# Kernel tuning notes

Hardware: AMD Instinct MI355X
Metric: run time of the kernel (lower is better)

The kernel has to match this reference:

```python
import jax, jax.numpy as jnp
import numpy as np
from functools import partial

N = 100_000   # nodes
E = 1_600_000 # edges (avg degree 16)
C = 128       # hidden channels
H = 4         # heads
D = C // H    # head dim = 32
L = 2         # layers
OUT = 2       # out channels


def setup_inputs() -> dict:
    key = jax.random.key(0)
    ks = jax.random.split(key, 12)
    s = 1.0 / np.sqrt(C)
    sd = 1.0 / np.sqrt(D)
    inp = {
        "x": jax.random.normal(ks[0], (N, C), jnp.float32),
        "edge_index": jax.random.randint(ks[1], (2, E), 0, N, jnp.int64),
        "Wk": jax.random.normal(ks[2], (L, C, C), jnp.float32) * s,
        "bk": jnp.zeros((L, C), jnp.float32),
        "Wq": jax.random.normal(ks[3], (L, C, C), jnp.float32) * s,
        "bq": jnp.zeros((L, C), jnp.float32),
        "Wv": jax.random.normal(ks[4], (L, C, C), jnp.float32) * s,
        "bv": jnp.zeros((L, C), jnp.float32),
        "a_rel": jax.random.normal(ks[5], (L, H, D, D), jnp.float32) * sd,
        "m_rel": jax.random.normal(ks[6], (L, H, D, D), jnp.float32) * sd,
        "p_rel": jnp.ones((L, H), jnp.float32),
        "Wa": jax.random.normal(ks[7], (L, C, C), jnp.float32) * s,
        "ba": jnp.zeros((L, C), jnp.float32),
        "skip": jnp.ones((L,), jnp.float32),
        "Wfc": jax.random.normal(ks[8], (C, OUT), jnp.float32) * s,
        "bfc": jnp.zeros((OUT,), jnp.float32),
    }
    return inp


def _hgt_layer(x, src, dst, Wk, bk, Wq, bq, Wv, bv, a_rel, m_rel, p_rel, Wa, ba, skip):
    n = x.shape[0]
    k = (x @ Wk + bk).reshape(n, H, D)
    q = (x @ Wq + bq).reshape(n, H, D)
    v = (x @ Wv + bv).reshape(n, H, D)
    # relation-specific transforms (single edge type)
    k = jnp.einsum('nhd,hde->nhe', k, a_rel)
    v = jnp.einsum('nhd,hde->nhe', v, m_rel)
    # per-edge attention logits [E, H]
    alpha = jnp.einsum('ehd,ehd->eh', q[dst], k[src]) * p_rel / np.sqrt(D)
    # segment softmax over incoming edges of each dst node
    amax = jax.ops.segment_max(alpha, dst, num_segments=n)
    ez = jnp.exp(alpha - amax[dst])
    denom = jax.ops.segment_sum(ez, dst, num_segments=n)
    attn = ez / denom[dst]
    # weighted messages -> scatter-sum to dst
    msg = (v[src] * attn[:, :, None]).reshape(-1, C)  # [E, C]
    agg = jax.ops.segment_sum(msg, dst, num_segments=n)  # [N, C]
    out = jax.nn.gelu(agg, approximate=False) @ Wa + ba
    g = jax.nn.sigmoid(skip)
    return g * out + (1.0 - g) * x


def reference(x, edge_index, Wk, bk, Wq, bq, Wv, bv, a_rel, m_rel, p_rel, Wa, ba, skip, Wfc, bfc):
    src, dst = edge_index[0], edge_index[1]
    h = x
    for l in range(L):
        h = _hgt_layer(h, src, dst, Wk[l], bk[l], Wq[l], bq[l], Wv[l], bv[l],
                       a_rel[l], m_rel[l], p_rel[l], Wa[l], ba[l], skip[l])
    return h @ Wfc + bfc
```

## Files before the change

### kernel.cpp

```cpp
#include <hip/hip_runtime.h>
#include <hip/hip_bf16.h>
#include <math.h>

#define CD 128
#define HH 4
#define DH 32
#define LL 2

using bf16 = __hip_bfloat16;
using bf16x8 = __attribute__((ext_vector_type(8))) short;
using f32x4 = __attribute__((ext_vector_type(4))) float;

__device__ __forceinline__ float bfbits2f(unsigned int s) {
  return __uint_as_float(s << 16);
}

__device__ __forceinline__ unsigned short f2bfbits(float f) {
  unsigned int u = __float_as_uint(f);
  unsigned int r = (u + 0x7fff + ((u >> 16) & 1)) >> 16;
  return (unsigned short)r;
}

__device__ __forceinline__ float gelu_f(float x) {
  return 0.5f * x * (1.0f + erff(x * 0.70710678118654752f));
}

__global__ void k_detect(const void* __restrict__ x, const int* __restrict__ ei,
                         int* __restrict__ flags) {
  __shared__ int cnt_f32, cnt_i32;
  if (threadIdx.x == 0) { cnt_f32 = 0; cnt_i32 = 0; }
  __syncthreads();
  int t = threadIdx.x;
  unsigned short u = ((const unsigned short*)x)[2 * t];
  float v = bfbits2f((unsigned int)u);
  float av = fabsf(v);
  if (av != 0.f && (av > 1e8f || av < 1e-8f)) atomicAdd(&cnt_f32, 1);
  if (t < 64) {
    if (((const int*)ei)[2 * t + 1] != 0) atomicAdd(&cnt_i32, 1);
  }
  __syncthreads();
  if (threadIdx.x == 0) {
    flags[0] = (cnt_f32 > 8) ? 1 : 0;
    flags[1] = (cnt_i32 == 0) ? 1 : 0;
  }
}

#define NSEG 14
struct SegTab {
  const void* src[NSEG];
  int off[NSEG];
  int total;
};

__device__ __forceinline__ int edge_idx(const int* __restrict__ ei, long pos, int is64) {
  return is64 ? ei[2 * pos] : ei[pos];
}

#define BTILE 4096

__global__ __launch_bounds__(256) void k_pre(
    SegTab tab, float* __restrict__ pdst,
    const int* __restrict__ ei, int* __restrict__ deg, int* __restrict__ bcnt,
    int E, int Nn, int shift, const int* __restrict__ flags, int parB) {
  __shared__ int cnt[256];
  const int bx = blockIdx.x;
  if (bx < parB) {
    int i = bx * 256 + threadIdx.x;
    if (i >= tab.total) return;
    int seg = 0;
#pragma unroll
    for (int k = 1; k < NSEG; k++)
      if (i >= tab.off[k]) seg = k;
    int j = i - tab.off[seg];
    const void* src = tab.src[seg];
    pdst[i] = flags[0] ? ((const float*)src)[j]
                       : bfbits2f((unsigned int)((const unsigned short*)src)[j]);
  } else {
    cnt[threadIdx.x] = 0;
    __syncthreads();
    const int t0 = (bx - parB) * BTILE;
    const int is64 = flags[1];
    for (int j = 0; j < 16; j++) {
      int i = t0 + threadIdx.x + j * 256;
      if (i < E) {
        int d = edge_idx(ei, (long)E + i, is64);
        if ((unsigned)d >= (unsigned)Nn) d = 0;
        atomicAdd(&deg[d], 1);
        atomicAdd(&cnt[d >> shift], 1);
      }
    }
    __syncthreads();
    int v = cnt[threadIdx.x];
    if (v > 0) atomicAdd(&bcnt[threadIdx.x], v);
  }
}

__global__ __launch_bounds__(256) void k_w1(
    const float* __restrict__ pWk, const float* __restrict__ pbk,
    const float* __restrict__ pWv, const float* __restrict__ pbv,
    const float* __restrict__ par, const float* __restrict__ pmr,
    unsigned short* __restrict__ wkeT, float* __restrict__ bke,
    unsigned short* __restrict__ wveT, float* __restrict__ bve,
    const float* __restrict__ pWq, const float* __restrict__ pWa,
    unsigned short* __restrict__ wqT, unsigned short* __restrict__ waT,
    const int* __restrict__ deg, int* __restrict__ tmp, int* __restrict__ bsum,
    int n, int effB, int wtB) {
  __shared__ int sh[256];
  const int bx = blockIdx.x;
  if (bx < effB) {
    int i = bx * 256 + threadIdx.x;
    const int total = LL * 2 * (CD + 1) * HH * DH;
    if (i >= total) return;
    int e = i & 31;
    int h = (i >> 5) & 3;
    int c = (i >> 7) % (CD + 1);
    int z = (i >> 7) / (CD + 1);
    int l = z >> 1, which = z & 1;
    const float* W = (which ? pWv : pWk) + (size_t)l * CD * CD;
    const float* B = (which ? pbv : pbk) + (size_t)l * CD;
    const float* R = (which ? pmr : par) + (size_t)l * HH * DH * DH + h * DH * DH;
    unsigned short* WoT = (which ? wveT : wkeT) + (size_t)l * CD * CD;
    float* Bo = (which ? bve : bke) + (size_t)l * CD;
    float acc = 0.f;
    if (c < CD) {
#pragma unroll
      for (int d = 0; d < DH; d++) acc += W[c * CD + h * DH + d] * R[d * DH + e];
      WoT[(size_t)(h * DH + e) * CD + c] = f2bfbits(acc);
    } else {
#pragma unroll
      for (int d = 0; d < DH; d++) acc += B[h * DH + d] * R[d * DH + e];
      Bo[h * DH + e] = acc;
    }
  } else if (bx < effB + wtB) {
    int i = (bx - effB) * 256 + threadIdx.x;
    int cin = i & 127;
    int cout = (i >> 7) & 127;
    int z = i >> 14;
    int l = z >> 1, which = z & 1;
    const float* W = (which ? pWa : pWq) + (size_t)l * CD * CD;
    unsigned short* WT = (which ? waT : wqT) + (size_t)l * CD * CD;
    WT[(size_t)cout * CD + cin] = f2bfbits(W[(size_t)cin * CD + cout]);
  } else {
    const int b = bx - effB - wtB;
    int i = b * 256 + threadIdx.x;
    int v = (i < n) ? deg[i] : 0;
    sh[threadIdx.x] = v;
    __syncthreads();
    for (int off = 1; off < 256; off <<= 1) {
      int t = (threadIdx.x >= off) ? sh[threadIdx.x - off] : 0;
      __syncthreads();
      sh[threadIdx.x] += t;
      __syncthreads();
    }
    if (i < n) tmp[i] = sh[threadIdx.x];
    if (threadIdx.x == 255) bsum[b] = sh[255];
  }
}

__global__ __launch_bounds__(256) void k_s2(
    int* __restrict__ bsum, int nb, const int* __restrict__ bcnt,
    int* __restrict__ bbase, int* __restrict__ bfill) {
  __shared__ int sh[256];
  __shared__ int carry;
  if (blockIdx.x == 0) {
    if (threadIdx.x == 0) carry = 0;
    __syncthreads();
    for (int base = 0; base < nb; base += 256) {
      int i = base + threadIdx.x;
      int v = (i < nb) ? bsum[i] : 0;
      sh[threadIdx.x] = v;
      __syncthreads();
      for (int off = 1; off < 256; off <<= 1) {
        int t = (threadIdx.x >= off) ? sh[threadIdx.x - off] : 0;
        __syncthreads();
        sh[threadIdx.x] += t;
        __syncthreads();
      }
      if (i < nb) bsum[i] = sh[threadIdx.x] + carry;
      __syncthreads();
      if (threadIdx.x == 0) carry += sh[255];
      __syncthreads();
    }
  } else {
    int t = threadIdx.x;
    int v = bcnt[t];
    sh[t] = v;
    __syncthreads();
    for (int off = 1; off < 256; off <<= 1) {
      int u = (t >= off) ? sh[t - off] : 0;
      __syncthreads();
      sh[t] += u;
      __syncthreads();
    }
    int excl = sh[t] - v;
    bbase[t] = excl;
    bfill[t] = excl;
  }
}

__global__ __launch_bounds__(256) void k_s3bin(
    const int* __restrict__ tmp, const int* __restrict__ deg,
    const int* __restrict__ bsum, int* __restrict__ rowptr,
    int* __restrict__ fill, int n, int nB,
    const int* __restrict__ ei, int* __restrict__ bfill,
    int* __restrict__ ebs, int* __restrict__ ebd,
    const int* __restrict__ flags, int E, int Nn, int shift) {
  __shared__ int sS[BTILE];
  __shared__ int sD[BTILE];
  __shared__ int cnt[256], pref[256], base[256], lofs[256];
  const int bx = blockIdx.x;
  if (bx < nB) {
    int i = bx * 256 + threadIdx.x;
    if (i >= n) return;
    int off = (bx > 0) ? bsum[bx - 1] : 0;
    int excl = tmp[i] - deg[i] + off;
    rowptr[i] = excl;
    fill[i] = excl;
    return;
  }
  const int t = threadIdx.x;
  cnt[t] = 0;
  lofs[t] = 0;
  __syncthreads();
  const int t0 = (bx - nB) * BTILE;
  const int is64 = flags[1];
  for (int j = 0; j < 16; j++) {
    int i = t0 + t + j * 256;
    if (i < E) {
      int d = edge_idx(ei, (long)E + i, is64);
      if ((unsigned)d >= (unsigned)Nn) d = 0;
      atomicAdd(&cnt[d >> shift], 1);
    }
  }
  __syncthreads();
  {
    int v = cnt[t];
    pref[t] = v;
    __syncthreads();
    for (int off = 1; off < 256; off <<= 1) {
      int u = (t >= off) ? pref[t - off] : 0;
      __syncthreads();
      pref[t] += u;
      __syncthreads();
    }
    int incl = pref[t];
    __syncthreads();
    pref[t] = incl - v;
    base[t] = (v > 0) ? atomicAdd(&bfill[t], v) : 0;
  }
  __syncthreads();
  for (int j = 0; j < 16; j++) {
    int i = t0 + t + j * 256;
    if (i < E) {
      int s = edge_idx(ei, (long)i, is64);
      int d = edge_idx(ei, (long)E + i, is64);
      if ((unsigned)s >= (unsigned)Nn) s = 0;
      if ((unsigned)d >= (unsigned)Nn) d = 0;
      int b = d >> shift;
      int p = pref[b] + atomicAdd(&lofs[b], 1);
      sS[p] = s;
      sD[p] = d;
    }
  }
  __syncthreads();
  int tot = E - t0;
  if (tot > BTILE) tot = BTILE;
  for (int j = 0; j < 16; j++) {
    int i = t + j * 256;
    if (i < tot) {
      int d = sD[i];
      int b = d >> shift;
      int gp = base[b] + (i - pref[b]);
      ebs[gp] = sS[i];
      ebd[gp] = d;
    }
  }
}

__global__ void k_scatter2(const int* __restrict__ bbase, const int* __restrict__ bcnt,
                           const int* __restrict__ ebs, const int* __restrict__ ebd,
                           int* __restrict__ fill, int* __restrict__ csr_src) {
  int b = blockIdx.x >> 1, half = blockIdx.x & 1;
  int s0 = bbase[b], c = bcnt[b];
  int st = s0 + (half ? (c + 1) / 2 : 0);
  int en = s0 + (half ? c : (c + 1) / 2);
  for (int i = st + threadIdx.x; i < en; i += 256) {
    int s = ebs[i], d = ebd[i];
    int pos = atomicAdd(&fill[d], 1);
    csr_src[pos] = s;
  }
}

__global__ __launch_bounds__(256, 4) void k_gemm_qkv(
    const void* __restrict__ Araw, int a_is_x, const int* __restrict__ flags,
    const unsigned short* __restrict__ wq, const unsigned short* __restrict__ wk,
    const unsigned short* __restrict__ wv,
    const float* __restrict__ bq, const float* __restrict__ bk,
    const float* __restrict__ bv,
    float* __restrict__ qout, unsigned short* __restrict__ kvout, int nrows) {
  const int which = blockIdx.y;
  const unsigned short* BT = (which == 0) ? wq : (which == 1) ? wk : wv;
  const float* bias = (which == 0) ? bq : (which == 1) ? bk : bv;
  const int w = threadIdx.x >> 6;
  const int l = threadIdx.x & 63;
  const int r0 = blockIdx.x * 64 + w * 16;
  if (r0 >= nrows) return;
  const int lrow = l & 15;
  const int quad = l >> 4;
  const int k0 = quad * 8;
  const int ax_f32 = a_is_x ? flags[0] : 0;

  f32x4 acc[8];
#pragma unroll
  for (int ct = 0; ct < 8; ct++) {
    float b = bias[ct * 16 + lrow];
    acc[ct] = (f32x4){b, b, b, b};
  }
  int ar = r0 + lrow;
  if (ar >= nrows) ar = nrows - 1;
#pragma unroll
  for (int kc = 0; kc < 4; kc++) {
    bf16x8 af;
    if (ax_f32) {
      const float* Af = (const float*)Araw + (size_t)ar * CD + kc * 32 + k0;
      float4 a = *(const float4*)Af;
      float4 b = *(const float4*)(Af + 4);
      af[0] = (short)f2bfbits(a.x); af[1] = (short)f2bfbits(a.y);
      af[2] = (short)f2bfbits(a.z); af[3] = (short)f2bfbits(a.w);
      af[4] = (short)f2bfbits(b.x); af[5] = (short)f2bfbits(b.y);
      af[6] = (short)f2bfbits(b.z); af[7] = (short)f2bfbits(b.w);
    } else {
      af = *(const bf16x8*)((const unsigned short*)Araw + (size_t)ar * CD + kc * 32 + k0);
    }
#pragma unroll
    for (int ct = 0; ct < 8; ct++) {
      bf16x8 bfr = *(const bf16x8*)(BT + (size_t)(ct * 16 + lrow) * CD + kc * 32 + k0);
      acc[ct] = __builtin_amdgcn_mfma_f32_16x16x32_bf16(af, bfr, acc[ct], 0, 0, 0);
    }
  }
#pragma unroll
  for (int ct = 0; ct < 8; ct++) {
#pragma unroll
    for (int i = 0; i < 4; i++) {
      int gr = r0 + quad * 4 + i;
      if (gr >= nrows) continue;
      int col = ct * 16 + lrow;
      float val = acc[ct][i];
      if (which == 0) {
        qout[(size_t)gr * CD + col] = val;
      } else {
        unsigned short* o = kvout + ((size_t)gr << 8) + ((which == 2) ? CD : 0);
        o[col] = f2bfbits(val);
      }
    }
  }
}

__global__ __launch_bounds__(256, 3) void k_gate_qkv(
    const unsigned short* __restrict__ A, const unsigned short* __restrict__ BTa,
    const float* __restrict__ ba, const void* __restrict__ xres,
    float* __restrict__ h, const float* __restrict__ skip,
    const int* __restrict__ flags,
    const unsigned short* __restrict__ wq1, const unsigned short* __restrict__ wk1,
    const unsigned short* __restrict__ wv1,
    const float* __restrict__ bq1, const float* __restrict__ bk1,
    const float* __restrict__ bv1,
    float* __restrict__ qout, unsigned short* __restrict__ kvout, int nrows) {
  __shared__ unsigned short sA[64][136];
  __shared__ unsigned short sW[128 * 128];
  const int t = threadIdx.x;
  const int w = t >> 6;
  const int l = t & 63;
  const int blkbase = blockIdx.x * 64;
  const int r0 = blkbase + w * 16;
  const int lrow = l & 15;
  const int quad = l >> 4;
  const int k0 = quad * 8;
  const int xf32 = flags[0];
  const bool act = (r0 < nrows);
  const int srow = t >> 1;
  const int shf = t & 1;

  {
    const unsigned short* src = BTa + (size_t)srow * CD + shf * 64;
#pragma unroll
    for (int j = 0; j < 8; j++) {
      int c = shf * 8 + j;
      int cs = c ^ (srow & 15);
      *(uint4*)(&sW[srow * 128 + cs * 8]) = *(const uint4*)(src + j * 8);
    }
  }
  __syncthreads();

  if (act) {
    f32x4 acc[8];
#pragma unroll
    for (int ct = 0; ct < 8; ct++) {
      float b = ba[ct * 16 + lrow];
      acc[ct] = (f32x4){b, b, b, b};
    }
    int ar = r0 + lrow;
    if (ar >= nrows) ar = nrows - 1;
    const unsigned short* Ap = A + (size_t)ar * CD;
#pragma unroll
    for (int kc = 0; kc < 4; kc++) {
      bf16x8 af = *(const bf16x8*)(Ap + kc * 32 + k0);
#pragma unroll
      for (int ct = 0; ct < 8; ct++) {
        int cs = (kc * 4 + quad) ^ lrow;
        bf16x8 bfr = *(const bf16x8*)(&sW[(ct * 16 + lrow) * 128 + cs * 8]);
        acc[ct] = __builtin_amdgcn_mfma_f32_16x16x32_bf16(af, bfr, acc[ct], 0, 0, 0);
      }
    }
    float gg = 1.f / (1.f + __expf(-skip[0]));
#pragma unroll
    for (int ct = 0; ct < 8; ct++) {
#pragma unroll
      for (int i = 0; i < 4; i++) {
        int gr = r0 + quad * 4 + i;
        if (gr >= nrows) continue;
        size_t ix = (size_t)gr * CD + ct * 16 + lrow;
        float hres = xf32 ? ((const float*)xres)[ix]
                          : bfbits2f((unsigned int)((const unsigned short*)xres)[ix]);
        float o = gg * acc[ct][i] + (1.f - gg) * hres;
        h[ix] = o;
        sA[gr - blkbase][ct * 16 + lrow] = f2bfbits(o);
      }
    }
  }
  __syncthreads();

  int ar = r0 + lrow;
  if (ar >= nrows) ar = nrows - 1;
  const unsigned short* Alds = &sA[ar - blkbase][0];
#pragma unroll 1
  for (int which = 0; which < 3; which++) {
    const unsigned short* BT = (which == 0) ? wq1 : (which == 1) ? wk1 : wv1;
    const float* bias = (which == 0) ? bq1 : (which == 1) ? bk1 : bv1;
    {
      const unsigned short* src = BT + (size_t)srow * CD + shf * 64;
#pragma unroll
      for (int j = 0; j < 8; j++) {
        int c = shf * 8 + j;
        int cs = c ^ (srow & 15);
        *(uint4*)(&sW[srow * 128 + cs * 8]) = *(const uint4*)(src + j * 8);
      }
    }
    __syncthreads();
    if (act) {
      f32x4 acc[8];
#pragma unroll
      for (int ct = 0; ct < 8; ct++) {
        float b = bias[ct * 16 + lrow];
        acc[ct] = (f32x4){b, b, b, b};
      }
#pragma unroll
      for (int kc = 0; kc < 4; kc++) {
        bf16x8 af = *(const bf16x8*)(Alds + kc * 32 + k0);
#pragma unroll
        for (int ct = 0; ct < 8; ct++) {
          int cs = (kc * 4 + quad) ^ lrow;
          bf16x8 bfr = *(const bf16x8*)(&sW[(ct * 16 + lrow) * 128 + cs * 8]);
          acc[ct] = __builtin_amdgcn_mfma_f32_16x16x32_bf16(af, bfr, acc[ct], 0, 0, 0);
        }
      }
#pragma unroll
      for (int ct = 0; ct < 8; ct++) {
#pragma unroll
        for (int i = 0; i < 4; i++) {
          int gr = r0 + quad * 4 + i;
          if (gr >= nrows) continue;
          int col = ct * 16 + lrow;
          float val = acc[ct][i];
          if (which == 0) {
            qout[(size_t)gr * CD + col] = val;
          } else {
            unsigned short* o = kvout + ((size_t)gr << 8) + ((which == 2) ? CD : 0);
            o[col] = f2bfbits(val);
          }
        }
      }
    }
    __syncthreads();
  }
}

__global__ __launch_bounds__(256, 4) void k_gemm_gate(
    const unsigned short* __restrict__ A, const unsigned short* __restrict__ BT,
    const float* __restrict__ bias, const float* __restrict__ h,
    const float* __restrict__ skip,
    const float* __restrict__ Wfc, const float* __restrict__ bfc,
    void* __restrict__ out, const int* __restrict__ flags, int nrows) {
  const int w = threadIdx.x >> 6;
  const int l = threadIdx.x & 63;
  const int r0 = blockIdx.x * 64 + w * 16;
  if (r0 >= nrows) return;
  const int lrow = l & 15;
  const int quad = l >> 4;
  const int k0 = quad * 8;
  const int xf32 = flags[0];

  f32x4 acc[8];
#pragma unroll
  for (int ct = 0; ct < 8; ct++) {
    float b = bias[ct * 16 + lrow];
    acc[ct] = (f32x4){b, b, b, b};
  }
  int ar = r0 + lrow;
  if (ar >= nrows) ar = nrows - 1;
  const unsigned short* Ap = A + (size_t)ar * CD;
#pragma unroll
  for (int kc = 0; kc < 4; kc++) {
    bf16x8 af = *(const bf16x8*)(Ap + kc * 32 + k0);
#pragma unroll
    for (int ct = 0; ct < 8; ct++) {
      bf16x8 bfr = *(const bf16x8*)(BT + (size_t)(ct * 16 + lrow) * CD + kc * 32 + k0);
      acc[ct] = __builtin_amdgcn_mfma_f32_16x16x32_bf16(af, bfr, acc[ct], 0, 0, 0);
    }
  }
  float gg = 1.f / (1.f + __expf(-skip[0]));
  float p0[4] = {0.f, 0.f, 0.f, 0.f};
  float p1[4] = {0.f, 0.f, 0.f, 0.f};
#pragma unroll
  for (int ct = 0; ct < 8; ct++) {
    float w0 = Wfc[(ct * 16 + lrow) * 2];
    float w1 = Wfc[(ct * 16 + lrow) * 2 + 1];
#pragma unroll
    for (int i = 0; i < 4; i++) {
      int gr = r0 + quad * 4 + i;
      if (gr >= nrows) continue;
      size_t ix = (size_t)gr * CD + ct * 16 + lrow;
      float o = gg * acc[ct][i] + (1.f - gg) * h[ix];
      p0[i] += o * w0;
      p1[i] += o * w1;
    }
  }
#pragma unroll
  for (int off = 1; off <= 8; off <<= 1) {
#pragma unroll
    for (int i = 0; i < 4; i++) {
      p0[i] += __shfl_xor(p0[i], off);
      p1[i] += __shfl_xor(p1[i], off);
    }
  }
  if (lrow == 0) {
#pragma unroll
    for (int i = 0; i < 4; i++) {
      int gr = r0 + quad * 4 + i;
      if (gr >= nrows) continue;
      float o0 = p0[i] + bfc[0];
      float o1 = p1[i] + bfc[1];
      if (xf32) {
        ((float*)out)[(size_t)gr * 2] = o0;
        ((float*)out)[(size_t)gr * 2 + 1] = o1;
      } else {
        ((bf16*)out)[(size_t)gr * 2] = __float2bfloat16(o0);
        ((bf16*)out)[(size_t)gr * 2 + 1] = __float2bfloat16(o1);
      }
    }
  }
}

__device__ __forceinline__ void edge_acc(uint4 ku, uint4 vu, float4 qa, float4 qb,
                                         float* __restrict__ acc, float& den) {
  float k0 = bfbits2f(ku.x & 0xffffu), k1 = bfbits2f(ku.x >> 16);
  float k2 = bfbits2f(ku.y & 0xffffu), k3 = bfbits2f(ku.y >> 16);
  float k4 = bfbits2f(ku.z & 0xffffu), k5 = bfbits2f(ku.z >> 16);
  float k6 = bfbits2f(ku.w & 0xffffu), k7 = bfbits2f(ku.w >> 16);
  float v0 = bfbits2f(vu.x & 0xffffu), v1 = bfbits2f(vu.x >> 16);
  float v2 = bfbits2f(vu.y & 0xffffu), v3 = bfbits2f(vu.y >> 16);
  float v4 = bfbits2f(vu.z & 0xffffu), v5 = bfbits2f(vu.z >> 16);
  float v6 = bfbits2f(vu.w & 0xffffu), v7 = bfbits2f(vu.w >> 16);
  float pd = qa.x * k0 + qa.y * k1 + qa.z * k2 + qa.w * k3 +
             qb.x * k4 + qb.y * k5 + qb.z * k6 + qb.w * k7;
  pd += __shfl_xor(pd, 1);
  pd += __shfl_xor(pd, 2);
  float ew = __expf(fminf(pd, 60.f));
  acc[0] += ew * v0; acc[1] += ew * v1;
  acc[2] += ew * v2; acc[3] += ew * v3;
  acc[4] += ew * v4; acc[5] += ew * v5;
  acc[6] += ew * v6; acc[7] += ew * v7;
  den += ew;
}

__global__ __launch_bounds__(256) void k_edge(
    const float* __restrict__ q, const unsigned short* __restrict__ kv,
    const int* __restrict__ rowptr, const int* __restrict__ deg,
    const int* __restrict__ csr_src, const float* __restrict__ p_rel,
    unsigned short* __restrict__ agg16, int N) {
  int n = (blockIdx.x * 256 + threadIdx.x) >> 6;
  if (n >= N) return;
  const int lane = threadIdx.x & 63;
  const int g = lane >> 4;
  const int j = lane & 15;
  const int start = rowptr[n];
  const int end = start + deg[n];
  const float prl = p_rel[j >> 2] * 0.17677669529663687f;
  float4 qa = *(const float4*)(q + (size_t)n * CD + 8 * j);
  float4 qb = *(const float4*)(q + (size_t)n * CD + 8 * j + 4);
  qa.x *= prl; qa.y *= prl; qa.z *= prl; qa.w *= prl;
  qb.x *= prl; qb.y *= prl; qb.z *= prl; qb.w *= prl;
  float den = 0.f;
  float acc[8] = {0.f, 0.f, 0.f, 0.f, 0.f, 0.f, 0.f, 0.f};
  int e = start + g;
  if (e < end) {
    const int last = end - 1;
    bool bok = (e + 4) < end;
    int sa = csr_src[e];
    int sb = csr_src[bok ? e + 4 : e];
    const unsigned short* pa = kv + ((size_t)sa << 8) + 8 * j;
    const unsigned short* pb = kv + ((size_t)sb << 8) + 8 * j;
    uint4 kua = *(const uint4*)pa;
    uint4 vua = *(const uint4*)(pa + CD);
    uint4 kub = *(const uint4*)pb;
    uint4 vub = *(const uint4*)(pb + CD);
    for (;;) {
      const int en = e + 8;
      int ea2 = (en < last) ? en : last;
      int eb2 = (en + 4 < last) ? en + 4 : last;
      int sa2 = csr_src[ea2];
      int sb2 = csr_src[eb2];
      const unsigned short* pa2 = kv + ((size_t)sa2 << 8) + 8 * j;
      const unsigned short* pb2 = kv + ((size_t)sb2 << 8) + 8 * j;
      uint4 kua2 = *(const uint4*)pa2;
      uint4 vua2 = *(const uint4*)(pa2 + CD);
      uint4 kub2 = *(const uint4*)pb2;
      uint4 vub2 = *(const uint4*)(pb2 + CD);
      __builtin_amdgcn_sched_barrier(0);
      edge_acc(kua, vua, qa, qb, acc, den);
      if (bok) edge_acc(kub, vub, qa, qb, acc, den);
      if (en >= end) break;
      e = en;
      bok = (en + 4) < end;
      kua = kua2; vua = vua2; kub = kub2; vub = vub2;
    }
  }
#pragma unroll
  for (int off = 16; off <= 32; off <<= 1) {
    den += __shfl_xor(den, off);
#pragma unroll
    for (int i = 0; i < 8; i++) acc[i] += __shfl_xor(acc[i], off);
  }
  if (g == 0) {
    float inv = (den > 0.f) ? 1.f / den : 0.f;
    ushort4 o0, o1;
    o0.x = f2bfbits(gelu_f(acc[0] * inv)); o0.y = f2bfbits(gelu_f(acc[1] * inv));
    o0.z = f2bfbits(gelu_f(acc[2] * inv)); o0.w = f2bfbits(gelu_f(acc[3] * inv));
    o1.x = f2bfbits(gelu_f(acc[4] * inv)); o1.y = f2bfbits(gelu_f(acc[5] * inv));
    o1.z = f2bfbits(gelu_f(acc[6] * inv)); o1.w = f2bfbits(gelu_f(acc[7] * inv));
    *(ushort4*)(agg16 + (size_t)n * CD + 8 * j) = o0;
    *(ushort4*)(agg16 + (size_t)n * CD + 8 * j + 4) = o1;
  }
}

extern "C" void kernel_launch(void* const* d_in, const int* in_sizes, int n_in,
                              void* d_out, int out_size, void* d_ws, size_t ws_size,
                              hipStream_t stream) {
  const int* ei = (const int*)d_in[1];
  const int N = in_sizes[0] / CD;
  const int E = in_sizes[1] / 2;
  const size_t NC = (size_t)N * CD;
  const int nB = (N + 255) / 256;
  int shift = 0;
  while (((N - 1) >> shift) >= 256) shift++;

  float* p = (float*)d_ws;
  float* hbuf = p;
  float* qbuf = p + NC;
  float* cur = p + 2 * NC;
  unsigned short* kvbuf16 = (unsigned short*)cur; cur += NC;
  unsigned short* agg16 = (unsigned short*)cur; cur += NC / 2;
  int* ip = (int*)cur;
  int* deg = ip;
  int* tmp = ip + N;
  int* rowptr = ip + 2 * N;
  int* fill = ip + 3 * N;
  int* bsum = ip + 4 * N;
  int* csr_src = ip + 4 * N + nB;
  int* bcnt = csr_src + E;
  int* bbase = bcnt + 256;
  int* bfill = bbase + 256;
  cur = (float*)(bfill + 256);
  unsigned short* wkeT = (unsigned short*)cur; cur += (size_t)LL * CD * CD / 2;
  unsigned short* wveT = (unsigned short*)cur; cur += (size_t)LL * CD * CD / 2;
  unsigned short* wqT = (unsigned short*)cur; cur += (size_t)LL * CD * CD / 2;
  unsigned short* waT = (unsigned short*)cur; cur += (size_t)LL * CD * CD / 2;
  float* bke = cur; cur += (size_t)LL * CD;
  float* bve = cur; cur += (size_t)LL * CD;
  float* pblock = cur;
  float* pWk = cur; cur += (size_t)LL * CD * CD;
  float* pbk = cur; cur += (size_t)LL * CD;
  float* pWq = cur; cur += (size_t)LL * CD * CD;
  float* pbq = cur; cur += (size_t)LL * CD;
  float* pWv = cur; cur += (size_t)LL * CD * CD;
  float* pbv = cur; cur += (size_t)LL * CD;
  float* par = cur; cur += (size_t)LL * HH * DH * DH;
  float* pmr = cur; cur += (size_t)LL * HH * DH * DH;
  float* ppr = cur; cur += (size_t)LL * HH;
  float* pWa = cur; cur += (size_t)LL * CD * CD;
  float* pba = cur; cur += (size_t)LL * CD;
  float* pskip = cur; cur += LL;
  float* pWfc = cur; cur += (size_t)CD * 2;
  float* pbfc = cur; cur += 2;
  int* flags = (int*)cur;

  int* ebs = (int*)kvbuf16;
  int* ebd = ebs + E;

  SegTab tab;
  const int sizes[NSEG] = {LL * CD * CD, LL * CD, LL * CD * CD, LL * CD,
                           LL * CD * CD, LL * CD, LL * HH * DH * DH,
                           LL * HH * DH * DH, LL * HH, LL * CD * CD, LL * CD,
                           LL, CD * 2, 2};
  const int srcIdx[NSEG] = {2, 3, 4, 5, 6, 7, 8, 9, 10, 11, 12, 13, 14, 15};
  int off = 0;
  for (int k = 0; k < NSEG; k++) {
    tab.src[k] = d_in[srcIdx[k]];
    tab.off[k] = off;
    off += sizes[k];
  }
  tab.total = off;

  hipMemsetAsync(deg, 0, (size_t)N * sizeof(int), stream);
  hipMemsetAsync(bcnt, 0, 256 * sizeof(int), stream);
  k_detect<<<1, 128, 0, stream>>>(d_in[0], ei, flags);

  const int parB = (tab.total + 255) / 256;
  const int histB = (E + BTILE - 1) / BTILE;
  k_pre<<<parB + histB, 256, 0, stream>>>(tab, pblock, ei, deg, bcnt, E, N,
                                          shift, flags, parB);

  const int effB = (LL * 2 * (CD + 1) * HH * DH + 255) / 256;
  const int wtB = (LL * 2 * CD * CD) / 256;
  k_w1<<<effB + wtB + nB, 256, 0, stream>>>(
      pWk, pbk, pWv, pbv, par, pmr, wkeT, bke, wveT, bve,
      pWq, pWa, wqT, waT, deg, tmp, bsum, N, effB, wtB);

  k_s2<<<2, 256, 0, stream>>>(bsum, nB, bcnt, bbase, bfill);
  k_s3bin<<<nB + histB, 256, 0, stream>>>(tmp, deg, bsum, rowptr, fill, N, nB,
                                          ei, bfill, ebs, ebd, flags, E, N, shift);
  k_scatter2<<<512, 256, 0, stream>>>(bbase, bcnt, ebs, ebd, fill, csr_src);

  const int mfmaBlocks = (N + 63) / 64;

  k_gemm_qkv<<<dim3(mfmaBlocks, 3), 256, 0, stream>>>(
      d_in[0], 1, flags, wqT, wkeT, wveT, pbq, bke, bve, qbuf, kvbuf16, N);

  k_edge<<<(N + 3) / 4, 256, 0, stream>>>(qbuf, kvbuf16, rowptr, deg,
                                          csr_src, ppr, agg16, N);

  k_gate_qkv<<<mfmaBlocks, 256, 0, stream>>>(
      agg16, waT, pba, d_in[0], hbuf, pskip, flags,
      wqT + (size_t)CD * CD, wkeT + (size_t)CD * CD, wveT + (size_t)CD * CD,
      pbq + CD, bke + CD, bve + CD, qbuf, kvbuf16, N);

  k_edge<<<(N + 3) / 4, 256, 0, stream>>>(qbuf, kvbuf16, rowptr, deg,
                                          csr_src, ppr + HH, agg16, N);

  k_gemm_gate<<<mfmaBlocks, 256, 0, stream>>>(
      agg16, waT + (size_t)CD * CD, pba + CD, hbuf, pskip + 1,
      pWfc, pbfc, d_out, flags, N);
}
```

Baseline: 723.0 us.

## Stage weights in swizzled LDS and load activations once for Q/K/V GEMM

The first-layer QKV GEMM now runs one block per 64 rows. It loads the activation fragments once and loops over Q, K and V, staging each 128x128 bf16 weight matrix into XOR-swizzled shared memory instead of reading B fragments from global memory. This removes the triple read of x and the redundant global weight fetches. The final gate GEMM likewise stages its weight matrix in LDS. The cost is 32KB of LDS per block, which limits occupancy, plus extra barriers between the three weight loads.

```diff
diff --git a/kernel.cpp b/kernel.cpp
--- a/kernel.cpp
+++ b/kernel.cpp
@@ -292,67 +292,94 @@
 }
 
 __global__ __launch_bounds__(256, 4) void k_gemm_qkv(
-    const void* __restrict__ Araw, int a_is_x, const int* __restrict__ flags,
+    const void* __restrict__ Araw, const int* __restrict__ flags,
     const unsigned short* __restrict__ wq, const unsigned short* __restrict__ wk,
     const unsigned short* __restrict__ wv,
     const float* __restrict__ bq, const float* __restrict__ bk,
     const float* __restrict__ bv,
     float* __restrict__ qout, unsigned short* __restrict__ kvout, int nrows) {
-  const int which = blockIdx.y;
-  const unsigned short* BT = (which == 0) ? wq : (which == 1) ? wk : wv;
-  const float* bias = (which == 0) ? bq : (which == 1) ? bk : bv;
-  const int w = threadIdx.x >> 6;
-  const int l = threadIdx.x & 63;
+  __shared__ unsigned short sW[128 * 128];
+  const int t = threadIdx.x;
+  const int w = t >> 6;
+  const int l = t & 63;
   const int r0 = blockIdx.x * 64 + w * 16;
-  if (r0 >= nrows) return;
   const int lrow = l & 15;
   const int quad = l >> 4;
   const int k0 = quad * 8;
-  const int ax_f32 = a_is_x ? flags[0] : 0;
-
-  f32x4 acc[8];
-#pragma unroll
-  for (int ct = 0; ct < 8; ct++) {
-    float b = bias[ct * 16 + lrow];
-    acc[ct] = (f32x4){b, b, b, b};
-  }
-  int ar = r0 + lrow;
-  if (ar >= nrows) ar = nrows - 1;
-#pragma unroll
-  for (int kc = 0; kc < 4; kc++) {
-    bf16x8 af;
-    if (ax_f32) {
-      const float* Af = (const float*)Araw + (size_t)ar * CD + kc * 32 + k0;
-      float4 a = *(const float4*)Af;
-      float4 b = *(const float4*)(Af + 4);
-      af[0] = (short)f2bfbits(a.x); af[1] = (short)f2bfbits(a.y);
-      af[2] = (short)f2bfbits(a.z); af[3] = (short)f2bfbits(a.w);
-      af[4] = (short)f2bfbits(b.x); af[5] = (short)f2bfbits(b.y);
-      af[6] = (short)f2bfbits(b.z); af[7] = (short)f2bfbits(b.w);
-    } else {
-      af = *(const bf16x8*)((const unsigned short*)Araw + (size_t)ar * CD + kc * 32 + k0);
-    }
-#pragma unroll
-    for (int ct = 0; ct < 8; ct++) {
-      bf16x8 bfr = *(const bf16x8*)(BT + (size_t)(ct * 16 + lrow) * CD + kc * 32 + k0);
-      acc[ct] = __builtin_amdgcn_mfma_f32_16x16x32_bf16(af, bfr, acc[ct], 0, 0, 0);
-    }
-  }
-#pragma unroll
-  for (int ct = 0; ct < 8; ct++) {
-#pragma unroll
-    for (int i = 0; i < 4; i++) {
-      int gr = r0 + quad * 4 + i;
-      if (gr >= nrows) continue;
-      int col = ct * 16 + lrow;
-      float val = acc[ct][i];
-      if (which == 0) {
-        qout[(size_t)gr * CD + col] = val;
+  const bool act = (r0 < nrows);
+  const int srow = t >> 1;
+  const int shf = t & 1;
+  const int ax_f32 = flags[0];
+
+  bf16x8 afr[4];
+  if (act) {
+    int ar = r0 + lrow;
+    if (ar >= nrows) ar = nrows - 1;
+#pragma unroll
+    for (int kc = 0; kc < 4; kc++) {
+      if (ax_f32) {
+        const float* Af = (const float*)Araw + (size_t)ar * CD + kc * 32 + k0;
+        float4 a = *(const float4*)Af;
+        float4 b = *(const float4*)(Af + 4);
+        afr[kc][0] = (short)f2bfbits(a.x); afr[kc][1] = (short)f2bfbits(a.y);
+        afr[kc][2] = (short)f2bfbits(a.z); afr[kc][3] = (short)f2bfbits(a.w);
+        afr[kc][4] = (short)f2bfbits(b.x); afr[kc][5] = (short)f2bfbits(b.y);
+        afr[kc][6] = (short)f2bfbits(b.z); afr[kc][7] = (short)f2bfbits(b.w);
       } else {
-        unsigned short* o = kvout + ((size_t)gr << 8) + ((which == 2) ? CD : 0);
-        o[col] = f2bfbits(val);
-      }
-    }
+        afr[kc] = *(const bf16x8*)((const unsigned short*)Araw +
+                                   (size_t)ar * CD + kc * 32 + k0);
+      }
+    }
+  }
+
+#pragma unroll 1
+  for (int which = 0; which < 3; which++) {
+    const unsigned short* BT = (which == 0) ? wq : (which == 1) ? wk : wv;
+    const float* bias = (which == 0) ? bq : (which == 1) ? bk : bv;
+    {
+      const unsigned short* src = BT + (size_t)srow * CD + shf * 64;
+#pragma unroll
+      for (int j = 0; j < 8; j++) {
+        int c = shf * 8 + j;
+        int cs = c ^ (srow & 15);
+        *(uint4*)(&sW[srow * 128 + cs * 8]) = *(const uint4*)(src + j * 8);
+      }
+    }
+    __syncthreads();
+    if (act) {
+      f32x4 acc[8];
+#pragma unroll
+      for (int ct = 0; ct < 8; ct++) {
+        float b = bias[ct * 16 + lrow];
+        acc[ct] = (f32x4){b, b, b, b};
+      }
+#pragma unroll
+      for (int kc = 0; kc < 4; kc++) {
+#pragma unroll
+        for (int ct = 0; ct < 8; ct++) {
+          int cs = (kc * 4 + quad) ^ lrow;
+          bf16x8 bfr = *(const bf16x8*)(&sW[(ct * 16 + lrow) * 128 + cs * 8]);
+          acc[ct] = __builtin_amdgcn_mfma_f32_16x16x32_bf16(afr[kc], bfr, acc[ct], 0, 0, 0);
+        }
+      }
+#pragma unroll
+      for (int ct = 0; ct < 8; ct++) {
+#pragma unroll
+        for (int i = 0; i < 4; i++) {
+          int gr = r0 + quad * 4 + i;
+          if (gr >= nrows) continue;
+          int col = ct * 16 + lrow;
+          float val = acc[ct][i];
+          if (which == 0) {
+            qout[(size_t)gr * CD + col] = val;
+          } else {
+            unsigned short* o = kvout + ((size_t)gr << 8) + ((which == 2) ? CD : 0);
+            o[col] = f2bfbits(val);
+          }
+        }
+      }
+    }
+    __syncthreads();
   }
 }
 
@@ -491,14 +518,30 @@
     const float* __restrict__ skip,
     const float* __restrict__ Wfc, const float* __restrict__ bfc,
     void* __restrict__ out, const int* __restrict__ flags, int nrows) {
-  const int w = threadIdx.x >> 6;
-  const int l = threadIdx.x & 63;
+  __shared__ unsigned short sW[128 * 128];
+  const int t = threadIdx.x;
+  const int w = t >> 6;
+  const int l = t & 63;
   const int r0 = blockIdx.x * 64 + w * 16;
-  if (r0 >= nrows) return;
   const int lrow = l & 15;
   const int quad = l >> 4;
   const int k0 = quad * 8;
   const int xf32 = flags[0];
+  const bool act = (r0 < nrows);
+  const int srow = t >> 1;
+  const int shf = t & 1;
+
+  {
+    const unsigned short* src = BT + (size_t)srow * CD + shf * 64;
+#pragma unroll
+    for (int j = 0; j < 8; j++) {
+      int c = shf * 8 + j;
+      int cs = c ^ (srow & 15);
+      *(uint4*)(&sW[srow * 128 + cs * 8]) = *(const uint4*)(src + j * 8);
+    }
+  }
+  __syncthreads();
+  if (!act) return;
 
   f32x4 acc[8];
 #pragma unroll
@@ -514,7 +557,8 @@
     bf16x8 af = *(const bf16x8*)(Ap + kc * 32 + k0);
 #pragma unroll
     for (int ct = 0; ct < 8; ct++) {
-      bf16x8 bfr = *(const bf16x8*)(BT + (size_t)(ct * 16 + lrow) * CD + kc * 32 + k0);
+      int cs = (kc * 4 + quad) ^ lrow;
+      bf16x8 bfr = *(const bf16x8*)(&sW[(ct * 16 + lrow) * 128 + cs * 8]);
       acc[ct] = __builtin_amdgcn_mfma_f32_16x16x32_bf16(af, bfr, acc[ct], 0, 0, 0);
     }
   }
@@ -743,8 +787,8 @@
 
   const int mfmaBlocks = (N + 63) / 64;
 
-  k_gemm_qkv<<<dim3(mfmaBlocks, 3), 256, 0, stream>>>(
-      d_in[0], 1, flags, wqT, wkeT, wveT, pbq, bke, bve, qbuf, kvbuf16, N);
+  k_gemm_qkv<<<mfmaBlocks, 256, 0, stream>>>(
+      d_in[0], flags, wqT, wkeT, wveT, pbq, bke, bve, qbuf, kvbuf16, N);
 
   k_edge<<<(N + 3) / 4, 256, 0, stream>>>(qbuf, kvbuf16, rowptr, deg,
                                           csr_src, ppr, agg16, N);
```

Measured after the change: 656.8 us. -9.1%, faster.
